# Kernel tuning notes

Measured on AMD Instinct MI355X. Metric: run time of the kernel, lower is better.

The kernel has to match this reference:

```python
import jax, jax.numpy as jnp
import numpy as np
import math

N_HEADS = 8
FACTOR = 5       # ProbSparse factor from DistSparseAtt(False, 5, ...)
LN_EPS = 1e-5


def _layer_norm(x, g, b):
    mu = x.mean(-1, keepdims=True)
    var = ((x - mu) ** 2).mean(-1, keepdims=True)
    return (x - mu) / jnp.sqrt(var + LN_EPS) * g + b


def _prob_sparse_attention(Q, K, V):
    # Informer-style ProbSparse attention, mask_flag=False, eval mode (no dropout).
    # Q, K, V: [B, H, L, Dh]
    B, H, L, Dh = Q.shape
    u = min(int(FACTOR * math.ceil(math.log(L))), L)  # sample_k == n_top (L_Q == L_K)
    # deterministic key sampling (torch.randint in the original)
    idx = jax.random.randint(jax.random.key(42), (L, u), 0, L)  # [L, u]
    K_samp = K[:, :, idx, :]                                    # [B,H,L,u,Dh]
    qk = jnp.einsum('bhld,bhlsd->bhls', Q, K_samp)              # [B,H,L,u]
    M = qk.max(-1) - qk.mean(-1)                                # sparsity measure [B,H,L]
    _, top = jax.lax.top_k(M, u)                                # [B,H,u] top-query indices
    Q_red = jnp.take_along_axis(Q, top[..., None], axis=2)      # [B,H,u,Dh]
    scale = 1.0 / jnp.sqrt(jnp.asarray(Dh, Q.dtype))
    scores = jnp.einsum('bhud,bhld->bhul', Q_red, K) * scale    # [B,H,u,L]
    attn = jax.nn.softmax(scores, axis=-1)
    upd = jnp.einsum('bhul,bhld->bhud', attn, V)                # [B,H,u,Dh]
    # initial context = mean of V over keys (mask_flag=False branch)
    ctx0 = jnp.broadcast_to(V.mean(axis=2, keepdims=True), Q.shape)
    ctx = jax.vmap(jax.vmap(lambda c, i, w: c.at[i].set(w)))(ctx0, top, upd)
    return ctx                                                  # [B,H,L,Dh]


def setup_inputs() -> dict:
    key = jax.random.key(0)
    ks = jax.random.split(key, 8)
    L, B, D, DFF = 1024, 4, 768, 2048
    return {
        'target': jax.random.normal(ks[0], (L, B, D), jnp.float32),
        'source': jax.random.normal(ks[1], (L, B, D), jnp.float32),
        'W1': jax.random.normal(ks[2], (DFF, D), jnp.float32) * 0.02,
        'b1': jax.random.normal(ks[3], (DFF,), jnp.float32) * 0.02,
        'W2': jax.random.normal(ks[4], (D, DFF), jnp.float32) * 0.02,
        'b2': jax.random.normal(ks[5], (D,), jnp.float32) * 0.02,
        'ln1_g': jnp.ones((D,), jnp.float32),
        'ln1_b': jnp.zeros((D,), jnp.float32),
        'ln2_g': jnp.ones((D,), jnp.float32),
        'ln2_b': jnp.zeros((D,), jnp.float32),
    }


def reference(target, source, W1, b1, W2, b2, ln1_g, ln1_b, ln2_g, ln2_b):
    L, B, Dm = target.shape
    Dh = Dm // N_HEADS
    # [L,B,Dm] -> [B,H,L,Dh]
    Q = jnp.transpose(target.reshape(L, B, N_HEADS, Dh), (1, 2, 0, 3))
    K = jnp.transpose(source.reshape(L, B, N_HEADS, Dh), (1, 2, 0, 3))
    ctx = _prob_sparse_attention(Q, K, K)                 # [B,H,L,Dh]
    attended = jnp.transpose(ctx, (2, 0, 1, 3)).reshape(L, B, Dm)
    normed1 = _layer_norm(target + attended, ln1_g, ln1_b)
    proj = jax.nn.relu(normed1 @ W1.T + b1) @ W2.T + b2
    return _layer_norm(normed1 + proj, ln2_g, ln2_b)
```

## Files before the change

kernel.cpp:

```cpp
#include <hip/hip_runtime.h>
#include <hip/hip_bf16.h>
#include <math.h>

#define L_SEQ 1024
#define BATCH 4
#define DMODEL 768
#define NH 8
#define DH 96
#define DFF 2048
#define U_TOP 35
#define NROWS (L_SEQ * BATCH)
#define NBH (BATCH * NH)
#define CHUNK 64
#define NCHUNK (L_SEQ / CHUNK)
#define VCH 64

typedef __attribute__((ext_vector_type(8))) short bf16x8;
typedef __attribute__((ext_vector_type(4))) float f32x4;

__device__ inline unsigned short f2bf(float f) {
  unsigned u = __float_as_uint(f);
  u += 0x7FFFu + ((u >> 16) & 1u);
  return (unsigned short)(u >> 16);
}

__device__ inline unsigned rotl32(unsigned v, int d) { return (v << d) | (v >> (32 - d)); }

__device__ inline void tf2x32(unsigned k0, unsigned k1, unsigned x0, unsigned x1,
                              unsigned& o0, unsigned& o1) {
  unsigned ks0 = k0, ks1 = k1, ks2 = k0 ^ k1 ^ 0x1BD11BDAu;
  x0 += ks0; x1 += ks1;
#define TFR(r) { x0 += x1; x1 = rotl32(x1, r); x1 ^= x0; }
  TFR(13) TFR(15) TFR(26) TFR(6)
  x0 += ks1; x1 += ks2 + 1u;
  TFR(17) TFR(29) TFR(16) TFR(24)
  x0 += ks2; x1 += ks0 + 2u;
  TFR(13) TFR(15) TFR(26) TFR(6)
  x0 += ks0; x1 += ks1 + 3u;
  TFR(17) TFR(29) TFR(16) TFR(24)
  x0 += ks1; x1 += ks2 + 4u;
  TFR(13) TFR(15) TFR(26) TFR(6)
  x0 += ks2; x1 += ks0 + 5u;
#undef TFR
  o0 = x0; o1 = x1;
}

__device__ inline int jax_randint1024(int j) {
  unsigned k2a, k2b, o0, o1;
  tf2x32(0u, 42u, 0u, 1u, k2a, k2b);
  tf2x32(k2a, k2b, 0u, (unsigned)j, o0, o1);
  return (int)((o0 ^ o1) & 1023u);
}

__global__ __launch_bounds__(256) void sample_scores(
    const float* __restrict__ target, const float* __restrict__ source,
    float* __restrict__ M) {
  int orig = blockIdx.x;
  int blk = (orig & 7) * (BATCH * L_SEQ / 8) + (orig >> 3);
  int l = blk & (L_SEQ - 1);
  int b = blk >> 10;
  __shared__ float qkbuf[NH][40];
  __shared__ int sidx[40];
  int tid = threadIdx.x;
  if (tid < 40) sidx[tid] = (tid < U_TOP) ? jax_randint1024(l * U_TOP + tid) : 0;
  int h = (tid >> 2) & 7, p = tid & 3;
  int s8 = tid >> 5;
  float4 qreg[6];
  {
    const float4* qg = (const float4*)(target + ((size_t)l * BATCH + b) * DMODEL + h * DH + p * 24);
#pragma unroll
    for (int j = 0; j < 6; ++j) qreg[j] = qg[j];
  }
  __syncthreads();
#pragma unroll
  for (int c = 0; c < 5; ++c) {
    int s = c * 8 + s8;
    if (s < U_TOP) {
      int kl = sidx[s];
      const float4* kg = (const float4*)(source + ((size_t)kl * BATCH + b) * DMODEL + h * DH + p * 24);
      float a = 0.f;
#pragma unroll
      for (int j = 0; j < 6; ++j) {
        float4 kv = kg[j];
        float4 qv = qreg[j];
        a += qv.x * kv.x + qv.y * kv.y + qv.z * kv.z + qv.w * kv.w;
      }
      a += __shfl_xor(a, 1, 64);
      a += __shfl_xor(a, 2, 64);
      if (p == 0) qkbuf[h][s] = a;
    }
  }
  __syncthreads();
  int w = tid >> 6, lane = tid & 63;
#pragma unroll
  for (int hi = 0; hi < 2; ++hi) {
    int hh = w * 2 + hi;
    float v = (lane < U_TOP) ? qkbuf[hh][lane] : -INFINITY;
    float sm = (lane < U_TOP) ? v : 0.f;
    float mx = v;
#pragma unroll
    for (int off = 32; off; off >>= 1) {
      mx = fmaxf(mx, __shfl_xor(mx, off, 64));
      sm += __shfl_xor(sm, off, 64);
    }
    if (lane == 0)
      M[(size_t)(b * NH + hh) * L_SEQ + l] = mx - sm * (1.f / U_TOP);
  }
}

__global__ __launch_bounds__(256) void topk_sel(const float* __restrict__ M,
                                                int* __restrict__ top, int* __restrict__ sel) {
  int bh = blockIdx.x;
  int tid = threadIdx.x;
  int lane = tid & 63, w = tid >> 6;
  __shared__ float wval[4];
  __shared__ int widx[4];
  __shared__ int bidx_sh;
  float v[4]; int ir[4];
#pragma unroll
  for (int i = 0; i < 4; ++i) {
    int ii = tid + i * 256;
    v[i] = M[(size_t)bh * L_SEQ + ii];
    ir[i] = ii;
    sel[(size_t)bh * L_SEQ + ii] = -1;
  }
  for (int it = 0; it < U_TOP; ++it) {
    float bv = v[0]; int bi = ir[0];
#pragma unroll
    for (int i = 1; i < 4; ++i)
      if (v[i] > bv || (v[i] == bv && ir[i] < bi)) { bv = v[i]; bi = ir[i]; }
#pragma unroll
    for (int off = 32; off; off >>= 1) {
      float ov = __shfl_xor(bv, off, 64);
      int oi = __shfl_xor(bi, off, 64);
      if (ov > bv || (ov == bv && oi < bi)) { bv = ov; bi = oi; }
    }
    if (lane == 0) { wval[w] = bv; widx[w] = bi; }
    __syncthreads();
    if (tid == 0) {
      float fv = wval[0]; int fi = widx[0];
#pragma unroll
      for (int k = 1; k < 4; ++k)
        if (wval[k] > fv || (wval[k] == fv && widx[k] < fi)) { fv = wval[k]; fi = widx[k]; }
      top[bh * U_TOP + it] = fi;
      sel[(size_t)bh * L_SEQ + fi] = it;
      bidx_sh = fi;
    }
    __syncthreads();
    int rb = bidx_sh;
    if ((rb & 255) == tid) v[rb >> 8] = -INFINITY;
  }
}

__global__ __launch_bounds__(768) void vmean_part(const float* __restrict__ source,
                                                  float* __restrict__ part) {
  int blk = blockIdx.x;
  int b = blk >> 6, c = blk & (VCH - 1);
  int d = threadIdx.x;
  float s = 0.f;
  int l0 = c * (L_SEQ / VCH);
#pragma unroll
  for (int l = l0; l < l0 + L_SEQ / VCH; ++l)
    s += source[((size_t)l * BATCH + b) * DMODEL + d];
  part[(size_t)blk * DMODEL + d] = s;
}

__global__ __launch_bounds__(768) void vmean_comb(const float* __restrict__ part,
                                                  float* __restrict__ vmean) {
  int b = blockIdx.x;
  int d = threadIdx.x;
  float s = 0.f;
  for (int c = 0; c < VCH; ++c) s += part[((size_t)(b * VCH + c)) * DMODEL + d];
  vmean[b * DMODEL + d] = s * (1.f / L_SEQ);
}

__global__ __launch_bounds__(256) void attn_flash(
    const float* __restrict__ target, const float* __restrict__ source,
    const int* __restrict__ top,
    float* __restrict__ part_O,
    float* __restrict__ part_m,
    float* __restrict__ part_s) {
  int blk = blockIdx.x;
  int chunk = blk & (NCHUNK - 1);
  int bh = blk >> 4;
  int h = bh & (NH - 1), b = bh >> 3;
  __shared__ short Qb[48 * 104];
  __shared__ short Kb[CHUNK * 104];
  __shared__ short Vt[96 * 72];
  __shared__ float sc[48 * 66];
  int tid = threadIdx.x;
  const float scale = 0.1020620726f;
  for (int i = tid; i < 13 * 104; i += 256) Qb[35 * 104 + i] = 0;
  for (int i = tid; i < U_TOP * 24; i += 256) {
    int u = i / 24, d4 = i - u * 24;
    int qpos = top[bh * U_TOP + u];
    float4 v = *(const float4*)(target + ((size_t)qpos * BATCH + b) * DMODEL + h * DH + d4 * 4);
    short* dst = Qb + u * 104 + d4 * 4;
    dst[0] = f2bf(v.x * scale); dst[1] = f2bf(v.y * scale);
    dst[2] = f2bf(v.z * scale); dst[3] = f2bf(v.w * scale);
  }
  int l0 = chunk * CHUNK;
  for (int i = tid; i < CHUNK * 24; i += 256) {
    int r = i / 24, d4 = i - r * 24;
    float4 v = *(const float4*)(source + ((size_t)(l0 + r) * BATCH + b) * DMODEL + h * DH + d4 * 4);
    short* dst = Kb + r * 104 + d4 * 4;
    dst[0] = f2bf(v.x); dst[1] = f2bf(v.y); dst[2] = f2bf(v.z); dst[3] = f2bf(v.w);
  }
  __syncthreads();
  for (int i = tid; i < CHUNK * 24; i += 256) {
    int r = i & (CHUNK - 1), d4 = i >> 6;
    const short* srcp = Kb + r * 104 + d4 * 4;
#pragma unroll
    for (int cc = 0; cc < 4; ++cc) Vt[(d4 * 4 + cc) * 72 + r] = srcp[cc];
  }
  int wv = tid >> 6, lane = tid & 63;
  int lr = lane & 15, lg = lane >> 4;
  __syncthreads();
  {
    int n = wv;
#pragma unroll
    for (int m = 0; m < 3; ++m) {
      f32x4 acc = {};
#pragma unroll
      for (int kc = 0; kc < 3; ++kc) {
        bf16x8 a = *(const bf16x8*)(Qb + (m * 16 + lr) * 104 + kc * 32 + lg * 8);
        bf16x8 bb = *(const bf16x8*)(Kb + (n * 16 + lr) * 104 + kc * 32 + lg * 8);
        acc = __builtin_amdgcn_mfma_f32_16x16x32_bf16(a, bb, acc, 0, 0, 0);
      }
#pragma unroll
      for (int j = 0; j < 4; ++j)
        sc[(m * 16 + lg * 4 + j) * 66 + n * 16 + lr] = acc[j];
    }
  }
  __syncthreads();
#pragma unroll
  for (int i = 0; i < 9; ++i) {
    int u = wv + 4 * i;
    if (u < U_TOP) {
      float s = sc[u * 66 + lane];
      float mx = s;
#pragma unroll
      for (int off = 32; off; off >>= 1) mx = fmaxf(mx, __shfl_xor(mx, off, 64));
      float pp = expf(s - mx);
      float sm = pp;
#pragma unroll
      for (int off = 32; off; off >>= 1) sm += __shfl_xor(sm, off, 64);
      Qb[u * 104 + lane] = f2bf(pp);
      if (lane == 0) {
        part_m[blk * U_TOP + u] = mx;
        part_s[blk * U_TOP + u] = sm;
      }
    }
  }
  __syncthreads();
  for (int t = wv; t < 18; t += 4) {
    int m = t / 6, n = t - (t / 6) * 6;
    f32x4 acc = {};
#pragma unroll
    for (int kc = 0; kc < 2; ++kc) {
      bf16x8 a = *(const bf16x8*)(Qb + (m * 16 + lr) * 104 + kc * 32 + lg * 8);
      bf16x8 bb = *(const bf16x8*)(Vt + (n * 16 + lr) * 72 + kc * 32 + lg * 8);
      acc = __builtin_amdgcn_mfma_f32_16x16x32_bf16(a, bb, acc, 0, 0, 0);
    }
#pragma unroll
    for (int j = 0; j < 4; ++j) {
      int u = m * 16 + lg * 4 + j;
      if (u < U_TOP)
        part_O[(size_t)blk * U_TOP * DH + u * DH + n * 16 + lr] = acc[j];
    }
  }
}

__global__ __launch_bounds__(256) void fuse_ln1(
    const float* __restrict__ target, const float* __restrict__ part_O,
    const float* __restrict__ part_m, const float* __restrict__ part_s,
    const int* __restrict__ sel, const float* __restrict__ vmean,
    const float* __restrict__ g, const float* __restrict__ bb,
    float* __restrict__ normed1, unsigned short* __restrict__ normed1b) {
  int r = blockIdx.x;
  int l = r >> 2, b = r & 3;
  __shared__ float wgt[NH][NCHUNK];
  __shared__ float sinv[NH];
  __shared__ int uarr[NH];
  __shared__ float x[DMODEL];
  __shared__ float red[256];
  int tid = threadIdx.x;
  if (tid < NH) uarr[tid] = sel[((size_t)(b * NH + tid)) * L_SEQ + l];
  __syncthreads();
  if (tid < NH * NCHUNK) {
    int h = tid >> 4, c = tid & 15;
    int u = uarr[h];
    if (u >= 0) {
      int bh = b * NH + h;
      float pm = part_m[(bh * NCHUNK + c) * U_TOP + u];
      float mx = pm;
#pragma unroll
      for (int off = 1; off < 16; off <<= 1) mx = fmaxf(mx, __shfl_xor(mx, off, 64));
      float wv = expf(pm - mx);
      float sv = wv * part_s[(bh * NCHUNK + c) * U_TOP + u];
#pragma unroll
      for (int off = 1; off < 16; off <<= 1) sv += __shfl_xor(sv, off, 64);
      wgt[h][c] = wv;
      if (c == 0) sinv[h] = 1.f / sv;
    }
  }
  __syncthreads();
  for (int d = tid; d < DMODEL; d += 256) {
    int h = d / DH;
    int u = uarr[h];
    float a;
    if (u >= 0) {
      int bh = b * NH + h;
      int dd = d - h * DH;
      float acc = 0.f;
#pragma unroll
      for (int c = 0; c < NCHUNK; ++c)
        acc += wgt[h][c] * part_O[((size_t)(bh * NCHUNK + c) * U_TOP + u) * DH + dd];
      a = acc * sinv[h];
    } else {
      a = vmean[b * DMODEL + d];
    }
    x[d] = target[(size_t)r * DMODEL + d] + a;
  }
  __syncthreads();
  float partial = 0.f;
  for (int d = tid; d < DMODEL; d += 256) partial += x[d];
  red[tid] = partial; __syncthreads();
  for (int s = 128; s; s >>= 1) { if (tid < s) red[tid] += red[tid + s]; __syncthreads(); }
  float mu = red[0] * (1.f / DMODEL);
  __syncthreads();
  partial = 0.f;
  for (int d = tid; d < DMODEL; d += 256) { float t = x[d] - mu; partial += t * t; }
  red[tid] = partial; __syncthreads();
  for (int s = 128; s; s >>= 1) { if (tid < s) red[tid] += red[tid + s]; __syncthreads(); }
  float rstd = 1.0f / sqrtf(red[0] * (1.f / DMODEL) + 1e-5f);
  for (int d = tid; d < DMODEL; d += 256) {
    float v = (x[d] - mu) * rstd * g[d] + bb[d];
    normed1[(size_t)r * DMODEL + d] = v;
    normed1b[(size_t)r * DMODEL + d] = f2bf(v);
  }
}

__global__ __launch_bounds__(256) void convert_bf16_2(
    const float* __restrict__ inA, const float* __restrict__ inB,
    unsigned short* __restrict__ outA, unsigned short* __restrict__ outB, int n4each) {
  int i = blockIdx.x * 256 + threadIdx.x;
  int stride = gridDim.x * 256;
  for (; i < 2 * n4each; i += stride) {
    const float* in = (i < n4each) ? inA : inB;
    unsigned short* outp = (i < n4each) ? outA : outB;
    int k = (i < n4each) ? i : i - n4each;
    float4 v = ((const float4*)in)[k];
    unsigned long long pk = (unsigned long long)f2bf(v.x)
                          | ((unsigned long long)f2bf(v.y) << 16)
                          | ((unsigned long long)f2bf(v.z) << 32)
                          | ((unsigned long long)f2bf(v.w) << 48);
    ((unsigned long long*)outp)[k] = pk;
  }
}

template <bool RELU, bool BF16OUT>
__global__ __launch_bounds__(256) void gemm_mfma64(
    const unsigned short* __restrict__ A, const unsigned short* __restrict__ B,
    const float* __restrict__ bias, void* __restrict__ Cout,
    int Ndim, int Kdim) {
  __shared__ short As[64 * 64];
  __shared__ short Bs[64 * 64];
  int tid = threadIdx.x;
  int lane = tid & 63;
  int wid = tid >> 6;
  int wm = wid >> 1, wn = wid & 1;
  int bm = blockIdx.y * 64, bn = blockIdx.x * 64;

  f32x4 acc[2][2] = {};

  for (int k0 = 0; k0 < Kdim; k0 += 64) {
#pragma unroll
    for (int i = 0; i < 2; ++i) {
      int trow = wid * 16 + i * 8 + (lane >> 3);
      int slot = (lane & 7) ^ (trow & 7);
      const unsigned short* ga = A + (size_t)(bm + trow) * Kdim + k0 + slot * 8;
      const unsigned short* gb = B + (size_t)(bn + trow) * Kdim + k0 + slot * 8;
      __builtin_amdgcn_global_load_lds(
          (const __attribute__((address_space(1))) void*)ga,
          (__attribute__((address_space(3))) void*)(As + (wid * 16 + i * 8) * 64),
          16, 0, 0);
      __builtin_amdgcn_global_load_lds(
          (const __attribute__((address_space(1))) void*)gb,
          (__attribute__((address_space(3))) void*)(Bs + (wid * 16 + i * 8) * 64),
          16, 0, 0);
    }
    __syncthreads();
#pragma unroll
    for (int c = 0; c < 2; ++c) {
      bf16x8 af[2], bf[2];
#pragma unroll
      for (int mi = 0; mi < 2; ++mi) {
        int row = wm * 32 + mi * 16 + (lane & 15);
        int phys = (c * 4 + (lane >> 4)) ^ (row & 7);
        af[mi] = *(const bf16x8*)(As + row * 64 + phys * 8);
      }
#pragma unroll
      for (int ni = 0; ni < 2; ++ni) {
        int row = wn * 32 + ni * 16 + (lane & 15);
        int phys = (c * 4 + (lane >> 4)) ^ (row & 7);
        bf[ni] = *(const bf16x8*)(Bs + row * 64 + phys * 8);
      }
#pragma unroll
      for (int mi = 0; mi < 2; ++mi)
#pragma unroll
        for (int ni = 0; ni < 2; ++ni)
          acc[mi][ni] = __builtin_amdgcn_mfma_f32_16x16x32_bf16(af[mi], bf[ni], acc[mi][ni], 0, 0, 0);
    }
    __syncthreads();
  }

#pragma unroll
  for (int mi = 0; mi < 2; ++mi)
#pragma unroll
    for (int ni = 0; ni < 2; ++ni) {
      int col = bn + wn * 32 + ni * 16 + (lane & 15);
      float bv = bias[col];
#pragma unroll
      for (int j = 0; j < 4; ++j) {
        int row = bm + wm * 32 + mi * 16 + (lane >> 4) * 4 + j;
        float v = acc[mi][ni][j] + bv;
        if (RELU) v = fmaxf(v, 0.f);
        if (BF16OUT)
          ((unsigned short*)Cout)[(size_t)row * Ndim + col] = f2bf(v);
        else
          ((float*)Cout)[(size_t)row * Ndim + col] = v;
      }
    }
}

__global__ __launch_bounds__(192) void ln2_out(
    const float* __restrict__ normed1, const float* __restrict__ proj,
    const float* __restrict__ g, const float* __restrict__ bb,
    float* __restrict__ out) {
  int r = blockIdx.x;
  int tid = threadIdx.x;
  __shared__ float red[6];
  float4 a = ((const float4*)(normed1 + (size_t)r * DMODEL))[tid];
  float4 p = ((const float4*)(proj + (size_t)r * DMODEL))[tid];
  float4 x = {a.x + p.x, a.y + p.y, a.z + p.z, a.w + p.w};
  float s1 = x.x + x.y + x.z + x.w;
  float s2 = x.x * x.x + x.y * x.y + x.z * x.z + x.w * x.w;
#pragma unroll
  for (int off = 32; off; off >>= 1) {
    s1 += __shfl_xor(s1, off, 64);
    s2 += __shfl_xor(s2, off, 64);
  }
  int w = tid >> 6;
  if ((tid & 63) == 0) { red[w] = s1; red[3 + w] = s2; }
  __syncthreads();
  float S1 = red[0] + red[1] + red[2];
  float S2 = red[3] + red[4] + red[5];
  float mu = S1 * (1.f / DMODEL);
  float var = S2 * (1.f / DMODEL) - mu * mu;
  float rstd = 1.0f / sqrtf(var + 1e-5f);
  float4 gv = ((const float4*)g)[tid];
  float4 bv = ((const float4*)bb)[tid];
  float4 o = {(x.x - mu) * rstd * gv.x + bv.x, (x.y - mu) * rstd * gv.y + bv.y,
              (x.z - mu) * rstd * gv.z + bv.z, (x.w - mu) * rstd * gv.w + bv.w};
  ((float4*)(out + (size_t)r * DMODEL))[tid] = o;
}

extern "C" void kernel_launch(void* const* d_in, const int* in_sizes, int n_in,
                              void* d_out, int out_size, void* d_ws, size_t ws_size,
                              hipStream_t stream) {
  const float* target = (const float*)d_in[0];
  const float* source = (const float*)d_in[1];
  const float* W1 = (const float*)d_in[2];
  const float* b1 = (const float*)d_in[3];
  const float* W2 = (const float*)d_in[4];
  const float* b2 = (const float*)d_in[5];
  const float* ln1_g = (const float*)d_in[6];
  const float* ln1_b = (const float*)d_in[7];
  const float* ln2_g = (const float*)d_in[8];
  const float* ln2_b = (const float*)d_in[9];
  float* out = (float*)d_out;

  char* ws = (char*)d_ws;
  float*          M        = (float*)         (ws + 0x0040000);
  int*            top      = (int*)           (ws + 0x0080000);
  int*            sel      = (int*)           (ws + 0x0090000);
  float*          vmean    = (float*)         (ws + 0x0130000);
  float*          part_m   = (float*)         (ws + 0x0140000);
  float*          part_s   = (float*)         (ws + 0x0160000);
  unsigned short* w1b      = (unsigned short*)(ws + 0x0180000);
  unsigned short* w2b      = (unsigned short*)(ws + 0x0480000);
  unsigned short* normed1b = (unsigned short*)(ws + 0x0780000);
  float*          normed1  = (float*)         (ws + 0x0D80000);
  unsigned short* h1b      = (unsigned short*)(ws + 0x1980000);
  float*          part_O   = (float*)         (ws + 0x1980000);
  float*          vpart    = (float*)         (ws + 0x2200000);
  float*          proj     = (float*)         (ws + 0x2980000);

  sample_scores<<<BATCH * L_SEQ, 256, 0, stream>>>(target, source, M);
  topk_sel<<<NBH, 256, 0, stream>>>(M, top, sel);
  vmean_part<<<BATCH * VCH, 768, 0, stream>>>(source, vpart);
  vmean_comb<<<BATCH, 768, 0, stream>>>(vpart, vmean);
  attn_flash<<<NBH * NCHUNK, 256, 0, stream>>>(target, source, top, part_O, part_m, part_s);
  convert_bf16_2<<<1024, 256, 0, stream>>>(W1, W2, w1b, w2b, DFF * DMODEL / 4);
  fuse_ln1<<<NROWS, 256, 0, stream>>>(target, part_O, part_m, part_s, sel, vmean,
                                      ln1_g, ln1_b, normed1, normed1b);
  {
    dim3 grid(DFF / 64, NROWS / 64);
    gemm_mfma64<true, true><<<grid, 256, 0, stream>>>(normed1b, w1b, b1, h1b, DFF, DMODEL);
  }
  {
    dim3 grid(DMODEL / 64, NROWS / 64);
    gemm_mfma64<false, false><<<grid, 256, 0, stream>>>(h1b, w2b, b2, proj, DMODEL, DFF);
  }
  ln2_out<<<NROWS, 192, 0, stream>>>(normed1, proj, ln2_g, ln2_b, out);
}
```

Measured before the change: 161.8 us.

## Merge independent kernels into shared launches and remap GEMM blocks across XCDs

The V-mean partial sums are folded into the sampling kernel, and the V-mean combine into the top-k kernel. The weight bf16 conversion becomes extra blocks of the attention kernel, so the launch count drops from ten to seven and independent work runs side by side. Both GEMMs now use a 1D grid whose block index is remapped so that neighbouring tiles land on the same XCD, aiming for better L2 reuse. The cost is that the fused kernels carry the shared-memory footprint and register pressure of the larger role, which can lower occupancy for the lighter work.

Result: faster. 148.9 us (-8.0%).

```diff
diff --git a/kernel.cpp b/kernel.cpp
--- a/kernel.cpp
+++ b/kernel.cpp
@@ -52,16 +52,31 @@
   return (int)((o0 ^ o1) & 1023u);
 }
 
-__global__ __launch_bounds__(256) void sample_scores(
+__global__ __launch_bounds__(256) void sample_vmean(
     const float* __restrict__ target, const float* __restrict__ source,
-    float* __restrict__ M) {
+    float* __restrict__ M, float* __restrict__ vpart) {
+  int tid = threadIdx.x;
+  if (blockIdx.x >= BATCH * L_SEQ) {
+    int blk = blockIdx.x - BATCH * L_SEQ;
+    int b = blk >> 6, c = blk & (VCH - 1);
+    int l0 = c * (L_SEQ / VCH);
+#pragma unroll
+    for (int k = 0; k < 3; ++k) {
+      int d = tid + k * 256;
+      float s = 0.f;
+#pragma unroll
+      for (int l = l0; l < l0 + L_SEQ / VCH; ++l)
+        s += source[((size_t)l * BATCH + b) * DMODEL + d];
+      vpart[(size_t)blk * DMODEL + d] = s;
+    }
+    return;
+  }
   int orig = blockIdx.x;
   int blk = (orig & 7) * (BATCH * L_SEQ / 8) + (orig >> 3);
   int l = blk & (L_SEQ - 1);
   int b = blk >> 10;
   __shared__ float qkbuf[NH][40];
   __shared__ int sidx[40];
-  int tid = threadIdx.x;
   if (tid < 40) sidx[tid] = (tid < U_TOP) ? jax_randint1024(l * U_TOP + tid) : 0;
   int h = (tid >> 2) & 7, p = tid & 3;
   int s8 = tid >> 5;
@@ -108,10 +123,22 @@
   }
 }
 
-__global__ __launch_bounds__(256) void topk_sel(const float* __restrict__ M,
-                                                int* __restrict__ top, int* __restrict__ sel) {
+__global__ __launch_bounds__(256) void topk_vmean(
+    const float* __restrict__ M, int* __restrict__ top, int* __restrict__ sel,
+    const float* __restrict__ vpart, float* __restrict__ vmean) {
+  int tid = threadIdx.x;
+  if (blockIdx.x >= NBH) {
+    int b = blockIdx.x - NBH;
+#pragma unroll
+    for (int k = 0; k < 3; ++k) {
+      int d = tid + k * 256;
+      float s = 0.f;
+      for (int c = 0; c < VCH; ++c) s += vpart[((size_t)(b * VCH + c)) * DMODEL + d];
+      vmean[b * DMODEL + d] = s * (1.f / L_SEQ);
+    }
+    return;
+  }
   int bh = blockIdx.x;
-  int tid = threadIdx.x;
   int lane = tid & 63, w = tid >> 6;
   __shared__ float wval[4];
   __shared__ int widx[4];
@@ -152,43 +179,38 @@
   }
 }
 
-__global__ __launch_bounds__(768) void vmean_part(const float* __restrict__ source,
-                                                  float* __restrict__ part) {
-  int blk = blockIdx.x;
-  int b = blk >> 6, c = blk & (VCH - 1);
-  int d = threadIdx.x;
-  float s = 0.f;
-  int l0 = c * (L_SEQ / VCH);
-#pragma unroll
-  for (int l = l0; l < l0 + L_SEQ / VCH; ++l)
-    s += source[((size_t)l * BATCH + b) * DMODEL + d];
-  part[(size_t)blk * DMODEL + d] = s;
-}
-
-__global__ __launch_bounds__(768) void vmean_comb(const float* __restrict__ part,
-                                                  float* __restrict__ vmean) {
-  int b = blockIdx.x;
-  int d = threadIdx.x;
-  float s = 0.f;
-  for (int c = 0; c < VCH; ++c) s += part[((size_t)(b * VCH + c)) * DMODEL + d];
-  vmean[b * DMODEL + d] = s * (1.f / L_SEQ);
-}
-
-__global__ __launch_bounds__(256) void attn_flash(
+__global__ __launch_bounds__(256) void attn_conv(
     const float* __restrict__ target, const float* __restrict__ source,
     const int* __restrict__ top,
-    float* __restrict__ part_O,
-    float* __restrict__ part_m,
-    float* __restrict__ part_s) {
-  int blk = blockIdx.x;
-  int chunk = blk & (NCHUNK - 1);
-  int bh = blk >> 4;
-  int h = bh & (NH - 1), b = bh >> 3;
+    float* __restrict__ part_O, float* __restrict__ part_m, float* __restrict__ part_s,
+    const float* __restrict__ W1, const float* __restrict__ W2,
+    unsigned short* __restrict__ w1b, unsigned short* __restrict__ w2b) {
   __shared__ short Qb[48 * 104];
   __shared__ short Kb[CHUNK * 104];
   __shared__ short Vt[96 * 72];
   __shared__ float sc[48 * 66];
   int tid = threadIdx.x;
+  if (blockIdx.x >= NBH * NCHUNK) {
+    const int n4each = DFF * DMODEL / 4;
+    int i = (blockIdx.x - NBH * NCHUNK) * 256 + tid;
+    int stride = 1024 * 256;
+    for (; i < 2 * n4each; i += stride) {
+      const float* in = (i < n4each) ? W1 : W2;
+      unsigned short* outp = (i < n4each) ? w1b : w2b;
+      int k = (i < n4each) ? i : i - n4each;
+      float4 v = ((const float4*)in)[k];
+      unsigned long long pk = (unsigned long long)f2bf(v.x)
+                            | ((unsigned long long)f2bf(v.y) << 16)
+                            | ((unsigned long long)f2bf(v.z) << 32)
+                            | ((unsigned long long)f2bf(v.w) << 48);
+      ((unsigned long long*)outp)[k] = pk;
+    }
+    return;
+  }
+  int blk = blockIdx.x;
+  int chunk = blk & (NCHUNK - 1);
+  int bh = blk >> 4;
+  int h = bh & (NH - 1), b = bh >> 3;
   const float scale = 0.1020620726f;
   for (int i = tid; i < 13 * 104; i += 256) Qb[35 * 104 + i] = 0;
   for (int i = tid; i < U_TOP * 24; i += 256) {
@@ -341,36 +363,21 @@
   }
 }
 
-__global__ __launch_bounds__(256) void convert_bf16_2(
-    const float* __restrict__ inA, const float* __restrict__ inB,
-    unsigned short* __restrict__ outA, unsigned short* __restrict__ outB, int n4each) {
-  int i = blockIdx.x * 256 + threadIdx.x;
-  int stride = gridDim.x * 256;
-  for (; i < 2 * n4each; i += stride) {
-    const float* in = (i < n4each) ? inA : inB;
-    unsigned short* outp = (i < n4each) ? outA : outB;
-    int k = (i < n4each) ? i : i - n4each;
-    float4 v = ((const float4*)in)[k];
-    unsigned long long pk = (unsigned long long)f2bf(v.x)
-                          | ((unsigned long long)f2bf(v.y) << 16)
-                          | ((unsigned long long)f2bf(v.z) << 32)
-                          | ((unsigned long long)f2bf(v.w) << 48);
-    ((unsigned long long*)outp)[k] = pk;
-  }
-}
-
 template <bool RELU, bool BF16OUT>
 __global__ __launch_bounds__(256) void gemm_mfma64(
     const unsigned short* __restrict__ A, const unsigned short* __restrict__ B,
     const float* __restrict__ bias, void* __restrict__ Cout,
-    int Ndim, int Kdim) {
+    int Ndim, int Kdim, int GX) {
   __shared__ short As[64 * 64];
   __shared__ short Bs[64 * 64];
   int tid = threadIdx.x;
   int lane = tid & 63;
   int wid = tid >> 6;
   int wm = wid >> 1, wn = wid & 1;
-  int bm = blockIdx.y * 64, bn = blockIdx.x * 64;
+  int nwg = gridDim.x;
+  int flat = (blockIdx.x & 7) * (nwg >> 3) + (blockIdx.x >> 3);
+  int bx = flat % GX, by = flat / GX;
+  int bm = by * 64, bn = bx * 64;
 
   f32x4 acc[2][2] = {};
 
@@ -497,21 +504,16 @@
   float*          vpart    = (float*)         (ws + 0x2200000);
   float*          proj     = (float*)         (ws + 0x2980000);
 
-  sample_scores<<<BATCH * L_SEQ, 256, 0, stream>>>(target, source, M);
-  topk_sel<<<NBH, 256, 0, stream>>>(M, top, sel);
-  vmean_part<<<BATCH * VCH, 768, 0, stream>>>(source, vpart);
-  vmean_comb<<<BATCH, 768, 0, stream>>>(vpart, vmean);
-  attn_flash<<<NBH * NCHUNK, 256, 0, stream>>>(target, source, top, part_O, part_m, part_s);
-  convert_bf16_2<<<1024, 256, 0, stream>>>(W1, W2, w1b, w2b, DFF * DMODEL / 4);
+  sample_vmean<<<BATCH * L_SEQ + BATCH * VCH, 256, 0, stream>>>(target, source, M, vpart);
+  topk_vmean<<<NBH + BATCH, 256, 0, stream>>>(M, top, sel, vpart, vmean);
+  attn_conv<<<NBH * NCHUNK + 1024, 256, 0, stream>>>(target, source, top,
+                                                     part_O, part_m, part_s,
+                                                     W1, W2, w1b, w2b);
   fuse_ln1<<<NROWS, 256, 0, stream>>>(target, part_O, part_m, part_s, sel, vmean,
                                       ln1_g, ln1_b, normed1, normed1b);
-  {
-    dim3 grid(DFF / 64, NROWS / 64);
-    gemm_mfma64<true, true><<<grid, 256, 0, stream>>>(normed1b, w1b, b1, h1b, DFF, DMODEL);
-  }
-  {
-    dim3 grid(DMODEL / 64, NROWS / 64);
-    gemm_mfma64<false, false><<<grid, 256, 0, stream>>>(h1b, w2b, b2, proj, DMODEL, DFF);
-  }
+  gemm_mfma64<true, true><<<(DFF / 64) * (NROWS / 64), 256, 0, stream>>>(
+      normed1b, w1b, b1, h1b, DFF, DMODEL, DFF / 64);
+  gemm_mfma64<false, false><<<(DMODEL / 64) * (NROWS / 64), 256, 0, stream>>>(
+      h1b, w2b, b2, proj, DMODEL, DFF, DMODEL / 64);
   ln2_out<<<NROWS, 192, 0, stream>>>(normed1, proj, ln2_g, ln2_b, out);
 }
```
